# Kernel optimization log

Measured on AMD Instinct MI355X. Metric: run time of the kernel, lower is better.

Reference implementation:

```python
import jax, jax.numpy as jnp
import numpy as np

B, T, V, D, L, FFM = 2, 2048, 50257, 1024, 8, 2


def setup_inputs() -> dict:
    key = jax.random.key(0)
    ks = jax.random.split(key, 10)
    s = 0.02
    return {
        "input_ids": jax.random.randint(ks[0], (B, T), 0, V),
        "embed": jax.random.normal(ks[1], (V, D), jnp.float32) * s,
        "norm1_w": jnp.ones((L, D), jnp.float32),
        "norm2_w": jnp.ones((L, D), jnp.float32),
        "a_diag": jax.random.uniform(ks[2], (L, D), jnp.float32, 0.5, 0.99),
        "W_in": jax.random.normal(ks[3], (L, D, D), jnp.float32) * s,
        "b_in": jnp.zeros((L, D), jnp.float32),
        "W_out": jax.random.normal(ks[4], (L, D, D), jnp.float32) * s,
        "ff_w1": jax.random.normal(ks[5], (L, D, FFM * D), jnp.float32) * s,
        "ff_b1": jnp.zeros((L, FFM * D), jnp.float32),
        "ff_w2": jax.random.normal(ks[6], (L, FFM * D, D), jnp.float32) * s,
        "ff_b2": jnp.zeros((L, D), jnp.float32),
        "final_norm_w": jnp.ones((D,), jnp.float32),
        "lm_head_w": jax.random.normal(ks[7], (V, D), jnp.float32) * s,
    }


def rmsnorm(x, w, eps=1e-6):
    return x * jax.lax.rsqrt(jnp.mean(x * x, axis=-1, keepdims=True) + eps) * w


def chaos_core(x, a, Win, bin_, Wout):
    pre = jnp.einsum('btd,de->bte', x, Win) + bin_  # precompute input drive (parallel)

    def step(s, p):
        s = jnp.tanh(a * s + p)
        return s, s

    s0 = jnp.zeros((x.shape[0], x.shape[-1]), x.dtype)
    _, hs = jax.lax.scan(step, s0, jnp.swapaxes(pre, 0, 1))  # (T, B, D)
    hs = jnp.swapaxes(hs, 0, 1)  # (B, T, D)
    return jnp.einsum('btd,de->bte', hs, Wout)


def reference(input_ids, embed, norm1_w, norm2_w, a_diag, W_in, b_in, W_out,
              ff_w1, ff_b1, ff_w2, ff_b2, final_norm_w, lm_head_w):
    x = embed[input_ids]  # (B, T, D)
    for i in range(L):
        # input_norm -> core -> residual
        x = x + chaos_core(rmsnorm(x, norm1_w[i]), a_diag[i], W_in[i], b_in[i], W_out[i])
        # ff_norm -> FeedForward (Linear -> SiLU -> Linear) -> residual
        h = rmsnorm(x, norm2_w[i])
        h = jax.nn.silu(jnp.einsum('btd,df->btf', h, ff_w1[i]) + ff_b1[i])
        x = x + jnp.einsum('btf,fd->btd', h, ff_w2[i]) + ff_b2[i]
    x = rmsnorm(x, final_norm_w)
    return jnp.einsum('btd,vd->btv', x, lm_head_w)  # logits (B, T, V)
```

## Files before the change

kernel.cpp:

```cpp
#include <hip/hip_runtime.h>

typedef unsigned short u16;
typedef __bf16 bf16x8 __attribute__((ext_vector_type(8)));
typedef float f32x4 __attribute__((ext_vector_type(4)));
typedef unsigned short u16x4 __attribute__((ext_vector_type(4)));

__device__ __forceinline__ u16 f2bf(float f) {
  union { float f; unsigned int u; } v; v.f = f;
  return (u16)((v.u + 0x7FFFu + ((v.u >> 16) & 1u)) >> 16);
}

__device__ __forceinline__ void gload16(const void* g, void* l) {
  __builtin_amdgcn_global_load_lds(
      (const __attribute__((address_space(1))) unsigned int*)g,
      (__attribute__((address_space(3))) unsigned int*)l, 16, 0, 0);
}

__global__ void prep_weights(const float* __restrict__ Win,
                             const float* __restrict__ Wout,
                             const float* __restrict__ ffw1,
                             const float* __restrict__ ffw2,
                             u16* __restrict__ WinT, u16* __restrict__ WoutT,
                             u16* __restrict__ f1T, u16* __restrict__ f2T) {
  __shared__ float tile[32][33];
  const int tk = blockIdx.x;
  const float* src; u16* dst;
  int R, C, tr, tc;
  if (tk < 8192) {
    const int l = tk >> 10, rem = tk & 1023;
    R = 1024; C = 1024; tr = rem >> 5; tc = rem & 31;
    src = Win + (size_t)l * 1048576; dst = WinT + (size_t)l * 1048576;
  } else if (tk < 16384) {
    const int q = tk - 8192, l = q >> 10, rem = q & 1023;
    R = 1024; C = 1024; tr = rem >> 5; tc = rem & 31;
    src = Wout + (size_t)l * 1048576; dst = WoutT + (size_t)l * 1048576;
  } else if (tk < 32768) {
    const int q = tk - 16384, l = q >> 11, rem = q & 2047;
    R = 1024; C = 2048; tr = rem >> 6; tc = rem & 63;
    src = ffw1 + (size_t)l * 2097152; dst = f1T + (size_t)l * 2097152;
  } else {
    const int q = tk - 32768, l = q >> 11, rem = q & 2047;
    R = 2048; C = 1024; tr = rem >> 5; tc = rem & 31;
    src = ffw2 + (size_t)l * 2097152; dst = f2T + (size_t)l * 2097152;
  }
  const int tx = threadIdx.x, ty = threadIdx.y;
  const int c0 = tc * 32, r0 = tr * 32;
#pragma unroll
  for (int k = 0; k < 32; k += 8)
    tile[ty + k][tx] = src[(size_t)(r0 + ty + k) * C + (c0 + tx)];
  __syncthreads();
#pragma unroll
  for (int k = 0; k < 32; k += 8)
    dst[(size_t)(c0 + ty + k) * R + (r0 + tx)] = f2bf(tile[tx][ty + k]);
}

__global__ void lm_cast_kernel(const float* __restrict__ lm, u16* __restrict__ out) {
  const int row = blockIdx.x;
  const int t = threadIdx.x;
  u16x4 o = {0, 0, 0, 0};
  if (row < 50257) {
    float4 v = *(const float4*)(lm + (size_t)row * 1024 + t * 4);
    o.x = f2bf(v.x); o.y = f2bf(v.y); o.z = f2bf(v.z); o.w = f2bf(v.w);
  }
  *(u16x4*)(out + (size_t)row * 1024 + t * 4) = o;
}

__global__ void embed_kernel(const int* __restrict__ ids, const float* __restrict__ embed,
                             float* __restrict__ x) {
  const int row = blockIdx.x;
  const int id = ids[row];
  const int t = threadIdx.x;
  *(float4*)(x + (size_t)row * 1024 + t * 4) =
      *(const float4*)(embed + (size_t)id * 1024 + t * 4);
}

__global__ void rmsnorm_kernel(const float* __restrict__ x, const float* __restrict__ w,
                               u16* __restrict__ out) {
  const int row = blockIdx.x, tid = threadIdx.x;
  const float* xr = x + (size_t)row * 1024;
  float4 v = *(const float4*)(xr + tid * 4);
  float ss = v.x * v.x + v.y * v.y + v.z * v.z + v.w * v.w;
#pragma unroll
  for (int off = 32; off; off >>= 1) ss += __shfl_xor(ss, off);
  __shared__ float red[4];
  if ((tid & 63) == 0) red[tid >> 6] = ss;
  __syncthreads();
  const float tot = red[0] + red[1] + red[2] + red[3];
  const float r = rsqrtf(tot * (1.0f / 1024.0f) + 1e-6f);
  float4 wv = *(const float4*)(w + tid * 4);
  u16x4 o;
  o.x = f2bf(v.x * r * wv.x); o.y = f2bf(v.y * r * wv.y);
  o.z = f2bf(v.z * r * wv.z); o.w = f2bf(v.w * r * wv.w);
  *(u16x4*)(out + (size_t)row * 1024 + tid * 4) = o;
}

__device__ __forceinline__ void sload(const float* __restrict__ p, int tb,
                                      float A2b, float (&buf)[8]) {
#pragma unroll
  for (int j = 0; j < 8; j++)
    buf[j] = fmaf(p[(size_t)(tb + j) * 1024], 2.8853900817779268f, A2b);
}

__device__ __forceinline__ void scomp(float (&buf)[8], float m2A2, float& r,
                                      u16* __restrict__ o, int tb) {
#pragma unroll
  for (int j = 0; j < 8; j++) {
    float z = fmaf(m2A2, r, buf[j]);
    float e = __builtin_amdgcn_exp2f(z);
    r = __builtin_amdgcn_rcpf(1.0f + e);
    o[(size_t)(tb + j) * 1024] = f2bf(fmaf(-2.0f, r, 1.0f));
  }
}

__global__ __launch_bounds__(256) void scan_kernel(const float* __restrict__ pre,
                                                   const float* __restrict__ a_diag,
                                                   const float* __restrict__ b_in,
                                                   u16* __restrict__ hs) {
  const int T = 2048;
  const int idx = blockIdx.x * 256 + threadIdx.x;
  const int b = idx >> 10, d = idx & 1023;
  const float* p = pre + (size_t)b * T * 1024 + d;
  u16* o = hs + (size_t)b * T * 1024 + d;
  const float A2 = a_diag[d] * 2.8853900817779268f;
  const float A2b = fmaf(2.8853900817779268f, b_in[d], A2);
  const float m2A2 = -2.0f * A2;
  float r = 0.5f;
  float b0[8], b1[8], b2[8], b3[8];
  sload(p, 0, A2b, b0); sload(p, 8, A2b, b1);
  sload(p, 16, A2b, b2); sload(p, 24, A2b, b3);
  for (int t0 = 0; t0 < T; t0 += 32) {
    scomp(b0, m2A2, r, o, t0);
    if (t0 + 32 < T) sload(p, t0 + 32, A2b, b0);
    scomp(b1, m2A2, r, o, t0 + 8);
    if (t0 + 32 < T) sload(p, t0 + 40, A2b, b1);
    scomp(b2, m2A2, r, o, t0 + 16);
    if (t0 + 32 < T) sload(p, t0 + 48, A2b, b2);
    scomp(b3, m2A2, r, o, t0 + 24);
    if (t0 + 32 < T) sload(p, t0 + 56, A2b, b3);
  }
}

template <int EPI>
__global__ __launch_bounds__(256) void gemmL(
    const u16* __restrict__ A, int lda, const u16* __restrict__ Bw, int ldb,
    const float* __restrict__ bias, float* Cf, u16* __restrict__ Cb,
    int ldc, int K) {
  __shared__ char lds[73728];
  const int tid = threadIdx.x;
  const int lane = tid & 63;
  const int wc = tid >> 6;
  const int tm = blockIdx.y * 64, tn = blockIdx.x * 128;
  const int lr = lane & 15;
  const int sb0 = ((lane >> 4) ^ (lane & 7)) << 4;

  const int srow = tid >> 3;
  const int sxs = ((tid & 7) ^ (srow & 7)) << 4;
  const char* pA = (const char*)A + (size_t)(tm + srow) * lda * 2 + sxs;
  const char* pB = (const char*)Bw + (size_t)(tn + srow) * ldb * 2 + sxs;
  const size_t a32 = (size_t)lda * 64;
  const size_t b32 = (size_t)ldb * 64;

#define STGL(kt, bufo)                                \
  {                                                   \
    char* d = lds + (bufo) + tid * 16;                \
    const size_t kb = (size_t)(kt) << 7;              \
    gload16(pA + kb, d);                              \
    gload16(pA + a32 + kb, d + 4096);                 \
    gload16(pB + kb, d + 8192);                       \
    gload16(pB + b32 + kb, d + 12288);                \
    gload16(pB + 2 * b32 + kb, d + 16384);            \
    gload16(pB + 3 * b32 + kb, d + 20480);            \
  }

  f32x4 acc[4][2] = {};
  const int nkt = K >> 6;

  STGL(0, 0);
  STGL(1, 24576);
  int cb = 0;
  for (int kt = 0; kt < nkt; ++kt) {
    if (kt + 2 < nkt) {
      const int nb = cb + 49152 >= 73728 ? cb - 24576 : cb + 49152;
      STGL(kt + 2, nb);
      asm volatile("s_waitcnt vmcnt(12)" ::: "memory");
    } else if (kt + 1 < nkt) {
      asm volatile("s_waitcnt vmcnt(6)" ::: "memory");
    } else {
      asm volatile("s_waitcnt vmcnt(0)" ::: "memory");
    }
    __builtin_amdgcn_s_barrier();
    const char* base = lds + cb;
    bf16x8 aF[4][2], bF[2][2];
#pragma unroll
    for (int m = 0; m < 4; m++)
#pragma unroll
      for (int ks = 0; ks < 2; ks++)
        aF[m][ks] =
            *(const bf16x8*)(base + (m * 16 + lr) * 128 + (sb0 ^ (ks << 6)));
#pragma unroll
    for (int n = 0; n < 2; n++)
#pragma unroll
      for (int ks = 0; ks < 2; ks++)
        bF[n][ks] = *(const bf16x8*)(base + 8192 +
                                     (wc * 32 + n * 16 + lr) * 128 +
                                     (sb0 ^ (ks << 6)));
#pragma unroll
    for (int ks = 0; ks < 2; ks++)
#pragma unroll
      for (int m = 0; m < 4; m++)
#pragma unroll
        for (int n = 0; n < 2; n++)
          acc[m][n] = __builtin_amdgcn_mfma_f32_16x16x32_bf16(
              aF[m][ks], bF[n][ks], acc[m][n], 0, 0, 0);
    __builtin_amdgcn_s_barrier();
    cb = (cb + 24576 == 73728) ? 0 : cb + 24576;
  }
#undef STGL

  const int crow = tm + ((lane >> 4) << 2);
  const int ccol = tn + wc * 32 + lr;
#pragma unroll
  for (int m = 0; m < 4; m++) {
#pragma unroll
    for (int n = 0; n < 2; n++) {
      const int cg = ccol + n * 16;
      float bb = 0.0f;
      if (EPI == 2 || EPI == 3) bb = bias[cg];
#pragma unroll
      for (int j = 0; j < 4; j++) {
        const size_t off = (size_t)(crow + m * 16 + j) * ldc + cg;
        const float v = acc[m][n][j] + bb;
        if (EPI == 0) {
          Cf[off] = v;
        } else if (EPI == 1) {
          Cf[off] += v;
        } else if (EPI == 2) {
          const float sg = __builtin_amdgcn_rcpf(
              1.0f + __builtin_amdgcn_exp2f(-1.4426950408889634f * v));
          Cb[off] = f2bf(v * sg);
        } else {
          Cf[off] += v;
        }
      }
    }
  }
}

__global__ __launch_bounds__(512, 2) void gemm_lm8(
    const u16* __restrict__ A, const u16* __restrict__ Bw,
    float* __restrict__ C, int Nreal) {
  __shared__ char lds[131072];
  const int tid = threadIdx.x;
  const int lane = tid & 63;
  const int wid = tid >> 6;
  const int wr = wid >> 2;
  const int wc = wid & 3;
  const int bid = blockIdx.x;
  const int tm = (((bid & 7) << 1) + ((bid >> 3) & 1)) << 8;
  const int tn = (bid >> 4) << 8;

  const int srow = tid >> 3;
  const int sxor = ((tid & 7) ^ (srow & 7)) << 4;
  const char* pAs = (const char*)A + ((size_t)(tm + srow) << 11) + sxor;
  const char* pBs = (const char*)Bw + ((size_t)(tn + srow) << 11) + sxor;

#define STG(p, h, kt, ro)                                      \
  {                                                            \
    char* d = lds + (ro) + tid * 16;                           \
    const char* s = (p) + ((size_t)(h) << 18) + ((kt) << 7);   \
    gload16(s, d);                                             \
    gload16(s + (64ull << 11), d + 8192);                      \
  }

  const int lr = lane & 15;
  const int sb0 = (((lane >> 4) ^ (lane & 7)) << 4);
  const int sb[2] = {sb0, sb0 ^ 64};
  const int aB = wr * 16384 + lr * 128;
  const int bB = 32768 + (wc >> 1) * 16384 + ((wc & 1) * 64 + lr) * 128;

  bf16x8 aR[4][2], bR[2][2][2];
  f32x4 acc[8][4] = {};

#define LDA_Q(bufo, mq)                                                         \
  _Pragma("unroll") for (int m_ = 0; m_ < 4; m_++)                              \
  _Pragma("unroll") for (int k_ = 0; k_ < 2; k_++)                              \
      aR[m_][k_] = *(const bf16x8*)(lds + (bufo) + aB + (mq)*8192 + m_*2048 + sb[k_]);

#define LDB_Q(bufo, nq)                                                         \
  _Pragma("unroll") for (int n_ = 0; n_ < 2; n_++)                              \
  _Pragma("unroll") for (int k_ = 0; k_ < 2; k_++)                              \
      bR[nq][n_][k_] = *(const bf16x8*)(lds + (bufo) + bB + (nq)*4096 + n_*2048 + sb[k_]);

#define MFMA_Q(mq, nq)                                                          \
  __builtin_amdgcn_s_setprio(1);                                                \
  _Pragma("unroll") for (int m_ = 0; m_ < 4; m_++)                              \
  _Pragma("unroll") for (int n_ = 0; n_ < 2; n_++)                              \
  _Pragma("unroll") for (int k_ = 0; k_ < 2; k_++)                              \
      acc[(mq)*4 + m_][(nq)*2 + n_] = __builtin_amdgcn_mfma_f32_16x16x32_bf16(  \
          aR[m_][k_], bR[nq][n_][k_], acc[(mq)*4 + m_][(nq)*2 + n_], 0, 0, 0);  \
  __builtin_amdgcn_s_setprio(0);

#define BAR() __builtin_amdgcn_s_barrier()
#define LGKM0() asm volatile("s_waitcnt lgkmcnt(0)" ::: "memory")

  STG(pAs, 0, 0, 0);
  STG(pAs, 1, 0, 16384);
  STG(pBs, 0, 0, 32768);
  STG(pBs, 1, 0, 49152);
  STG(pBs, 0, 1, 65536 + 32768);
  STG(pBs, 1, 1, 65536 + 49152);
  asm volatile("s_waitcnt vmcnt(4)" ::: "memory");
  BAR();

  for (int it = 0; it < 8; ++it) {
    const int t1 = 2 * it + 1, t2 = 2 * it + 2, t3 = 2 * it + 3;
    const bool st = (it < 7);
    LDA_Q(0, 0); LDB_Q(0, 0);
    STG(pAs, 0, t1, 65536);
    BAR(); LGKM0(); MFMA_Q(0, 0); BAR();
    LDB_Q(0, 1);
    STG(pAs, 1, t1, 65536 + 16384);
    BAR(); LGKM0(); MFMA_Q(0, 1); BAR();
    LDA_Q(0, 1);
    if (st) STG(pBs, 0, t2, 32768);
    BAR(); LGKM0(); MFMA_Q(1, 0); BAR();
    if (st) STG(pBs, 1, t2, 49152);
    BAR(); LGKM0(); MFMA_Q(1, 1);
    if (st) { asm volatile("s_waitcnt vmcnt(4)" ::: "memory"); }
    else    { asm volatile("s_waitcnt vmcnt(0)" ::: "memory"); }
    BAR();
    LDA_Q(65536, 0); LDB_Q(65536, 0);
    if (st) STG(pAs, 0, t2, 0);
    BAR(); LGKM0(); MFMA_Q(0, 0); BAR();
    LDB_Q(65536, 1);
    if (st) STG(pAs, 1, t2, 16384);
    BAR(); LGKM0(); MFMA_Q(0, 1); BAR();
    LDA_Q(65536, 1);
    if (st) STG(pBs, 0, t3, 65536 + 32768);
    BAR(); LGKM0(); MFMA_Q(1, 0); BAR();
    if (st) STG(pBs, 1, t3, 65536 + 49152);
    BAR(); LGKM0(); MFMA_Q(1, 1);
    if (st) { asm volatile("s_waitcnt vmcnt(4)" ::: "memory"); }
    else    { asm volatile("s_waitcnt vmcnt(0)" ::: "memory"); }
    BAR();
  }
#undef STG
#undef LDA_Q
#undef LDB_Q
#undef MFMA_Q
#undef BAR
#undef LGKM0

  const int crow = tm + wr * 128 + ((lane >> 4) << 2);
  const int ccol = tn + wc * 64 + lr;
#pragma unroll
  for (int M_ = 0; M_ < 8; M_++) {
    const int r = crow + (M_ >> 2) * 64 + (M_ & 3) * 16;
#pragma unroll
    for (int N_ = 0; N_ < 4; N_++) {
      const int cg = ccol + (N_ >> 1) * 32 + (N_ & 1) * 16;
      if (cg < Nreal) {
#pragma unroll
        for (int j = 0; j < 4; j++)
          C[(size_t)(r + j) * Nreal + cg] = acc[M_][N_][j];
      }
    }
  }
}

extern "C" void kernel_launch(void* const* d_in, const int* in_sizes, int n_in,
                              void* d_out, int out_size, void* d_ws, size_t ws_size,
                              hipStream_t stream) {
  const int D = 1024, V = 50257, L = 8;
  const int M = 4096;
  const int Vpad = 50432;
  const size_t MD = (size_t)M * D;

  const int* ids = (const int*)d_in[0];
  const float* embedw = (const float*)d_in[1];
  const float* norm1_w = (const float*)d_in[2];
  const float* norm2_w = (const float*)d_in[3];
  const float* a_diag = (const float*)d_in[4];
  const float* W_in = (const float*)d_in[5];
  const float* b_in = (const float*)d_in[6];
  const float* W_out = (const float*)d_in[7];
  const float* ff_w1 = (const float*)d_in[8];
  const float* ff_b1 = (const float*)d_in[9];
  const float* ff_w2 = (const float*)d_in[10];
  const float* ff_b2 = (const float*)d_in[11];
  const float* final_norm_w = (const float*)d_in[12];
  const float* lm_head_w = (const float*)d_in[13];

  char* w = (char*)d_ws;
  float* x = (float*)w;   w += MD * 4;
  u16* h = (u16*)w;       w += MD * 2;
  float* pre = (float*)w; w += MD * 4;
  u16* hs = (u16*)w;      w += MD * 2;
  u16* hff = (u16*)w;     w += MD * 2 * 2;
  u16* WinT = (u16*)w;    w += (size_t)L * D * D * 2;
  u16* WoutT = (u16*)w;   w += (size_t)L * D * D * 2;
  u16* ffw1T = (u16*)w;   w += (size_t)L * 2 * D * D * 2;
  u16* ffw2T = (u16*)w;   w += (size_t)L * 2 * D * D * 2;
  u16* lmpad = (u16*)w;   w += (size_t)Vpad * D * 2;

  prep_weights<<<49152, dim3(32, 8), 0, stream>>>(
      W_in, W_out, ff_w1, ff_w2, WinT, WoutT, ffw1T, ffw2T);
  lm_cast_kernel<<<Vpad, 256, 0, stream>>>(lm_head_w, lmpad);
  embed_kernel<<<M, 256, 0, stream>>>(ids, embedw, x);

  for (int l = 0; l < L; l++) {
    rmsnorm_kernel<<<M, 256, 0, stream>>>(x, norm1_w + (size_t)l * D, h);
    gemmL<0><<<dim3(8, 64), 256, 0, stream>>>(
        h, D, WinT + (size_t)l * D * D, D, nullptr, pre, nullptr, D, D);
    scan_kernel<<<8, 256, 0, stream>>>(pre, a_diag + (size_t)l * D,
                                       b_in + (size_t)l * D, hs);
    gemmL<1><<<dim3(8, 64), 256, 0, stream>>>(
        hs, D, WoutT + (size_t)l * D * D, D, nullptr, x, nullptr, D, D);
    rmsnorm_kernel<<<M, 256, 0, stream>>>(x, norm2_w + (size_t)l * D, h);
    gemmL<2><<<dim3(16, 64), 256, 0, stream>>>(
        h, D, ffw1T + (size_t)l * 2 * D * D, D, ff_b1 + (size_t)l * 2 * D,
        nullptr, hff, 2 * D, D);
    gemmL<3><<<dim3(8, 64), 256, 0, stream>>>(
        hff, 2 * D, ffw2T + (size_t)l * 2 * D * D, 2 * D,
        ff_b2 + (size_t)l * D, x, nullptr, D, 2 * D);
  }

  rmsnorm_kernel<<<M, 256, 0, stream>>>(x, final_norm_w, h);
  gemm_lm8<<<dim3(8 * 394), 512, 0, stream>>>(h, lmpad, (float*)d_out, V);
}
```

Baseline: 2.712 ms.

## Fuse per-layer kernels into one persistent cooperative megakernel with grid syncs

Replaces the per-layer sequence of rmsnorm, GEMM and scan launches with a single cooperative kernel of 256 blocks. It runs the embedding, lm_head cast, norms, GEMMs with 128x128 tiles and the scan as phases separated by grid.sync. The aim is to remove many kernel launch gaps. In exchange, the GEMMs now use only 256 persistent blocks with double buffering, and the scan runs on 4 blocks while the rest wait at a barrier. The fallback gemmL also drops from triple to double buffering.

```diff
diff --git a/kernel.cpp b/kernel.cpp
--- a/kernel.cpp
+++ b/kernel.cpp
@@ -1,4 +1,7 @@
 #include <hip/hip_runtime.h>
+#include <hip/hip_cooperative_groups.h>
+
+namespace cg = cooperative_groups;
 
 typedef unsigned short u16;
 typedef __bf16 bf16x8 __attribute__((ext_vector_type(8)));
@@ -112,32 +115,35 @@
   }
 }
 
-__global__ __launch_bounds__(256) void scan_kernel(const float* __restrict__ pre,
-                                                   const float* __restrict__ a_diag,
-                                                   const float* __restrict__ b_in,
-                                                   u16* __restrict__ hs) {
-  const int T = 2048;
-  const int idx = blockIdx.x * 256 + threadIdx.x;
-  const int b = idx >> 10, d = idx & 1023;
-  const float* p = pre + (size_t)b * T * 1024 + d;
-  u16* o = hs + (size_t)b * T * 1024 + d;
-  const float A2 = a_diag[d] * 2.8853900817779268f;
-  const float A2b = fmaf(2.8853900817779268f, b_in[d], A2);
+__device__ __forceinline__ void scan_chain(const float* __restrict__ p,
+                                           u16* __restrict__ o, float A2,
+                                           float A2b) {
   const float m2A2 = -2.0f * A2;
   float r = 0.5f;
   float b0[8], b1[8], b2[8], b3[8];
   sload(p, 0, A2b, b0); sload(p, 8, A2b, b1);
   sload(p, 16, A2b, b2); sload(p, 24, A2b, b3);
-  for (int t0 = 0; t0 < T; t0 += 32) {
+  for (int t0 = 0; t0 < 2048; t0 += 32) {
     scomp(b0, m2A2, r, o, t0);
-    if (t0 + 32 < T) sload(p, t0 + 32, A2b, b0);
+    if (t0 + 32 < 2048) sload(p, t0 + 32, A2b, b0);
     scomp(b1, m2A2, r, o, t0 + 8);
-    if (t0 + 32 < T) sload(p, t0 + 40, A2b, b1);
+    if (t0 + 32 < 2048) sload(p, t0 + 40, A2b, b1);
     scomp(b2, m2A2, r, o, t0 + 16);
-    if (t0 + 32 < T) sload(p, t0 + 48, A2b, b2);
+    if (t0 + 32 < 2048) sload(p, t0 + 48, A2b, b2);
     scomp(b3, m2A2, r, o, t0 + 24);
-    if (t0 + 32 < T) sload(p, t0 + 56, A2b, b3);
-  }
+    if (t0 + 32 < 2048) sload(p, t0 + 56, A2b, b3);
+  }
+}
+
+__global__ __launch_bounds__(256) void scan_kernel(const float* __restrict__ pre,
+                                                   const float* __restrict__ a_diag,
+                                                   const float* __restrict__ b_in,
+                                                   u16* __restrict__ hs) {
+  const int idx = blockIdx.x * 256 + threadIdx.x;
+  const int b = idx >> 10, d = idx & 1023;
+  const float A2 = a_diag[d] * 2.8853900817779268f;
+  const float A2b = fmaf(2.8853900817779268f, b_in[d], A2);
+  scan_chain(pre + (size_t)b * 2097152 + d, hs + (size_t)b * 2097152 + d, A2, A2b);
 }
 
 template <int EPI>
@@ -145,7 +151,7 @@
     const u16* __restrict__ A, int lda, const u16* __restrict__ Bw, int ldb,
     const float* __restrict__ bias, float* Cf, u16* __restrict__ Cb,
     int ldc, int K) {
-  __shared__ char lds[73728];
+  __shared__ char lds[49152];
   const int tid = threadIdx.x;
   const int lane = tid & 63;
   const int wc = tid >> 6;
@@ -176,20 +182,16 @@
   const int nkt = K >> 6;
 
   STGL(0, 0);
-  STGL(1, 24576);
-  int cb = 0;
+  int cur = 0;
   for (int kt = 0; kt < nkt; ++kt) {
-    if (kt + 2 < nkt) {
-      const int nb = cb + 49152 >= 73728 ? cb - 24576 : cb + 49152;
-      STGL(kt + 2, nb);
-      asm volatile("s_waitcnt vmcnt(12)" ::: "memory");
-    } else if (kt + 1 < nkt) {
+    if (kt + 1 < nkt) {
+      STGL(kt + 1, (cur ^ 1) * 24576);
       asm volatile("s_waitcnt vmcnt(6)" ::: "memory");
     } else {
       asm volatile("s_waitcnt vmcnt(0)" ::: "memory");
     }
     __builtin_amdgcn_s_barrier();
-    const char* base = lds + cb;
+    const char* base = lds + cur * 24576;
     bf16x8 aF[4][2], bF[2][2];
 #pragma unroll
     for (int m = 0; m < 4; m++)
@@ -213,7 +215,7 @@
           acc[m][n] = __builtin_amdgcn_mfma_f32_16x16x32_bf16(
               aF[m][ks], bF[n][ks], acc[m][n], 0, 0, 0);
     __builtin_amdgcn_s_barrier();
-    cb = (cb + 24576 == 73728) ? 0 : cb + 24576;
+    cur ^= 1;
   }
 #undef STGL
 
@@ -244,6 +246,195 @@
       }
     }
   }
+}
+
+
+template <int EPI>
+__device__ __forceinline__ void gemm_phase(
+    char* lds, const u16* __restrict__ A, int lda,
+    const u16* __restrict__ B, int ldb, const float* __restrict__ bias,
+    float* __restrict__ Cf, u16* __restrict__ Cb, int ldc,
+    int ntm, int ntn, int K) {
+  const int tid = threadIdx.x;
+  const int lane = tid & 63;
+  const int wid = tid >> 6;
+  const int wr = wid >> 2, wc = wid & 3;
+  const int lr = lane & 15;
+  const int sb0 = ((lane >> 4) ^ (lane & 7)) << 4;
+  const int srow = tid >> 3;
+  const int sxs = ((tid & 7) ^ (srow & 7)) << 4;
+  const int nkt = K >> 6;
+  const int ntiles = ntm * ntn;
+
+  for (int t = blockIdx.x; t < ntiles; t += gridDim.x) {
+    const int tm = (t / ntn) << 7, tn = (t % ntn) << 7;
+    const char* pA = (const char*)A + (size_t)(tm + srow) * lda * 2 + sxs;
+    const char* pB = (const char*)B + (size_t)(tn + srow) * ldb * 2 + sxs;
+    const size_t pA2 = (size_t)lda << 7;
+    const size_t pB2 = (size_t)ldb << 7;
+    f32x4 acc[4][2] = {};
+    __syncthreads();
+    {
+      char* d = lds + tid * 16;
+      gload16(pA, d); gload16(pA + pA2, d + 8192);
+      gload16(pB, d + 16384); gload16(pB + pB2, d + 24576);
+    }
+    int cur = 0;
+    for (int kt = 0; kt < nkt; ++kt) {
+      if (kt + 1 < nkt) {
+        const size_t kb = (size_t)(kt + 1) << 7;
+        char* d = lds + (cur ^ 1) * 32768 + tid * 16;
+        gload16(pA + kb, d); gload16(pA + pA2 + kb, d + 8192);
+        gload16(pB + kb, d + 16384); gload16(pB + pB2 + kb, d + 24576);
+        asm volatile("s_waitcnt vmcnt(4)" ::: "memory");
+      } else {
+        asm volatile("s_waitcnt vmcnt(0)" ::: "memory");
+      }
+      __builtin_amdgcn_s_barrier();
+      const char* base = lds + cur * 32768;
+      bf16x8 aF[4][2], bF[2][2];
+#pragma unroll
+      for (int m = 0; m < 4; m++)
+#pragma unroll
+        for (int ks = 0; ks < 2; ks++)
+          aF[m][ks] = *(const bf16x8*)(base + (wr * 64 + m * 16 + lr) * 128 +
+                                       (sb0 ^ (ks << 6)));
+#pragma unroll
+      for (int n = 0; n < 2; n++)
+#pragma unroll
+        for (int ks = 0; ks < 2; ks++)
+          bF[n][ks] = *(const bf16x8*)(base + 16384 +
+                                       (wc * 32 + n * 16 + lr) * 128 +
+                                       (sb0 ^ (ks << 6)));
+#pragma unroll
+      for (int ks = 0; ks < 2; ks++)
+#pragma unroll
+        for (int m = 0; m < 4; m++)
+#pragma unroll
+          for (int n = 0; n < 2; n++)
+            acc[m][n] = __builtin_amdgcn_mfma_f32_16x16x32_bf16(
+                aF[m][ks], bF[n][ks], acc[m][n], 0, 0, 0);
+      __builtin_amdgcn_s_barrier();
+      cur ^= 1;
+    }
+    const int crow = tm + wr * 64 + ((lane >> 4) << 2);
+    const int ccol = tn + wc * 32 + lr;
+#pragma unroll
+    for (int m = 0; m < 4; m++) {
+#pragma unroll
+      for (int n = 0; n < 2; n++) {
+        const int cg = ccol + n * 16;
+#pragma unroll
+        for (int j = 0; j < 4; j++) {
+          const size_t off = (size_t)(crow + m * 16 + j) * ldc + cg;
+          const float v = acc[m][n][j];
+          if (EPI == 0) {
+            Cf[off] = v;
+          } else if (EPI == 1) {
+            Cf[off] += v;
+          } else if (EPI == 2) {
+            const float vb = v + bias[cg];
+            const float sg = __builtin_amdgcn_rcpf(
+                1.0f + __builtin_amdgcn_exp2f(-1.4426950408889634f * vb));
+            Cb[off] = f2bf(vb * sg);
+          } else {
+            Cf[off] += v + bias[cg];
+          }
+        }
+      }
+    }
+  }
+}
+
+__device__ __forceinline__ void norm_phase(const float* __restrict__ xg,
+                                           const float* __restrict__ w,
+                                           u16* __restrict__ hg,
+                                           volatile float* red) {
+  const int tid = threadIdx.x;
+  const int sub = tid >> 8, t = tid & 255;
+#pragma unroll 1
+  for (int i = 0; i < 8; i++) {
+    const int row = blockIdx.x * 16 + i * 2 + sub;
+    const size_t ro = (size_t)row * 1024 + t * 4;
+    float4 v = *(const float4*)(xg + ro);
+    float ss = v.x * v.x + v.y * v.y + v.z * v.z + v.w * v.w;
+#pragma unroll
+    for (int off = 32; off; off >>= 1) ss += __shfl_xor(ss, off);
+    __syncthreads();
+    if ((tid & 63) == 0) red[tid >> 6] = ss;
+    __syncthreads();
+    const float tot =
+        red[sub * 4] + red[sub * 4 + 1] + red[sub * 4 + 2] + red[sub * 4 + 3];
+    const float rr = rsqrtf(tot * (1.0f / 1024.0f) + 1e-6f);
+    float4 wv = *(const float4*)(w + t * 4);
+    u16x4 o;
+    o.x = f2bf(v.x * rr * wv.x); o.y = f2bf(v.y * rr * wv.y);
+    o.z = f2bf(v.z * rr * wv.z); o.w = f2bf(v.w * rr * wv.w);
+    *(u16x4*)(hg + ro) = o;
+  }
+}
+
+__global__ __launch_bounds__(512, 1) void mega(
+    const int* __restrict__ ids, const float* __restrict__ embedw,
+    const float* __restrict__ n1w, const float* __restrict__ n2w,
+    const float* __restrict__ adiag, const float* __restrict__ bin,
+    const float* __restrict__ fb1, const float* __restrict__ fb2,
+    const float* __restrict__ finw, const float* __restrict__ lmw,
+    float* __restrict__ x, u16* __restrict__ h, float* __restrict__ pre,
+    u16* __restrict__ hs, u16* __restrict__ hff,
+    const u16* __restrict__ WinT, const u16* __restrict__ WoutT,
+    const u16* __restrict__ f1T, const u16* __restrict__ f2T,
+    u16* __restrict__ lmpad) {
+  __shared__ char smem[65536];
+  __shared__ float red[16];
+  cg::grid_group grid = cg::this_grid();
+  const int bid = blockIdx.x;
+  const int tid = threadIdx.x;
+
+  for (int row = bid; row < 50432; row += 256) {
+    unsigned int o = 0;
+    if (row < 50257) {
+      float2 v = *(const float2*)(lmw + (size_t)row * 1024 + tid * 2);
+      o = (unsigned int)f2bf(v.x) | ((unsigned int)f2bf(v.y) << 16);
+    }
+    *(unsigned int*)(lmpad + (size_t)row * 1024 + tid * 2) = o;
+  }
+  for (int row = bid; row < 4096; row += 256) {
+    const float2 v =
+        *(const float2*)(embedw + (size_t)ids[row] * 1024 + tid * 2);
+    *(float2*)(x + (size_t)row * 1024 + tid * 2) = v;
+  }
+  grid.sync();
+
+  for (int l = 0; l < 8; ++l) {
+    norm_phase(x, n1w + l * 1024, h, red);
+    grid.sync();
+    gemm_phase<0>(smem, h, 1024, WinT + (size_t)l * 1048576, 1024, nullptr,
+                  pre, nullptr, 1024, 32, 8, 1024);
+    grid.sync();
+    if (bid < 4) {
+      const int idx = bid * 512 + tid;
+      const int b = idx >> 10, d = idx & 1023;
+      const float A2 = adiag[l * 1024 + d] * 2.8853900817779268f;
+      const float A2b = fmaf(2.8853900817779268f, bin[l * 1024 + d], A2);
+      scan_chain(pre + (size_t)b * 2097152 + d, hs + (size_t)b * 2097152 + d,
+                 A2, A2b);
+    }
+    grid.sync();
+    gemm_phase<1>(smem, hs, 1024, WoutT + (size_t)l * 1048576, 1024, nullptr,
+                  x, nullptr, 1024, 32, 8, 1024);
+    grid.sync();
+    norm_phase(x, n2w + l * 1024, h, red);
+    grid.sync();
+    gemm_phase<2>(smem, h, 1024, f1T + (size_t)l * 2097152, 1024,
+                  fb1 + l * 2048, nullptr, hff, 2048, 32, 16, 1024);
+    grid.sync();
+    gemm_phase<3>(smem, hff, 2048, f2T + (size_t)l * 2097152, 2048,
+                  fb2 + l * 1024, x, nullptr, 1024, 32, 8, 2048);
+    grid.sync();
+  }
+
+  norm_phase(x, finw, h, red);
 }
 
 __global__ __launch_bounds__(512, 2) void gemm_lm8(
@@ -405,26 +596,37 @@
 
   prep_weights<<<49152, dim3(32, 8), 0, stream>>>(
       W_in, W_out, ff_w1, ff_w2, WinT, WoutT, ffw1T, ffw2T);
-  lm_cast_kernel<<<Vpad, 256, 0, stream>>>(lm_head_w, lmpad);
-  embed_kernel<<<M, 256, 0, stream>>>(ids, embedw, x);
-
-  for (int l = 0; l < L; l++) {
-    rmsnorm_kernel<<<M, 256, 0, stream>>>(x, norm1_w + (size_t)l * D, h);
-    gemmL<0><<<dim3(8, 64), 256, 0, stream>>>(
-        h, D, WinT + (size_t)l * D * D, D, nullptr, pre, nullptr, D, D);
-    scan_kernel<<<8, 256, 0, stream>>>(pre, a_diag + (size_t)l * D,
-                                       b_in + (size_t)l * D, hs);
-    gemmL<1><<<dim3(8, 64), 256, 0, stream>>>(
-        hs, D, WoutT + (size_t)l * D * D, D, nullptr, x, nullptr, D, D);
-    rmsnorm_kernel<<<M, 256, 0, stream>>>(x, norm2_w + (size_t)l * D, h);
-    gemmL<2><<<dim3(16, 64), 256, 0, stream>>>(
-        h, D, ffw1T + (size_t)l * 2 * D * D, D, ff_b1 + (size_t)l * 2 * D,
-        nullptr, hff, 2 * D, D);
-    gemmL<3><<<dim3(8, 64), 256, 0, stream>>>(
-        hff, 2 * D, ffw2T + (size_t)l * 2 * D * D, 2 * D,
-        ff_b2 + (size_t)l * D, x, nullptr, D, 2 * D);
-  }
-
-  rmsnorm_kernel<<<M, 256, 0, stream>>>(x, final_norm_w, h);
+
+  void* args[] = {
+      (void*)&ids,  (void*)&embedw, (void*)&norm1_w, (void*)&norm2_w,
+      (void*)&a_diag, (void*)&b_in, (void*)&ff_b1,   (void*)&ff_b2,
+      (void*)&final_norm_w, (void*)&lm_head_w,
+      (void*)&x, (void*)&h, (void*)&pre, (void*)&hs, (void*)&hff,
+      (void*)&WinT, (void*)&WoutT, (void*)&ffw1T, (void*)&ffw2T,
+      (void*)&lmpad};
+  hipError_t err = hipLaunchCooperativeKernel((const void*)mega, dim3(256),
+                                              dim3(512), args, 0, stream);
+  if (err != hipSuccess) {
+    lm_cast_kernel<<<Vpad, 256, 0, stream>>>(lm_head_w, lmpad);
+    embed_kernel<<<M, 256, 0, stream>>>(ids, embedw, x);
+    for (int l = 0; l < L; l++) {
+      rmsnorm_kernel<<<M, 256, 0, stream>>>(x, norm1_w + (size_t)l * D, h);
+      gemmL<0><<<dim3(8, 64), 256, 0, stream>>>(
+          h, D, WinT + (size_t)l * D * D, D, nullptr, pre, nullptr, D, D);
+      scan_kernel<<<8, 256, 0, stream>>>(pre, a_diag + (size_t)l * D,
+                                         b_in + (size_t)l * D, hs);
+      gemmL<1><<<dim3(8, 64), 256, 0, stream>>>(
+          hs, D, WoutT + (size_t)l * D * D, D, nullptr, x, nullptr, D, D);
+      rmsnorm_kernel<<<M, 256, 0, stream>>>(x, norm2_w + (size_t)l * D, h);
+      gemmL<2><<<dim3(16, 64), 256, 0, stream>>>(
+          h, D, ffw1T + (size_t)l * 2 * D * D, D, ff_b1 + (size_t)l * 2 * D,
+          nullptr, hff, 2 * D, D);
+      gemmL<3><<<dim3(8, 64), 256, 0, stream>>>(
+          hff, 2 * D, ffw2T + (size_t)l * 2 * D * D, 2 * D,
+          ff_b2 + (size_t)l * D, x, nullptr, D, 2 * D);
+    }
+    rmsnorm_kernel<<<M, 256, 0, stream>>>(x, final_norm_w, h);
+  }
+
   gemm_lm8<<<dim3(8 * 394), 512, 0, stream>>>(h, lmpad, (float*)d_out, V);
 }
```

After: 5.971 ms. +120.2%, slower.

## Merge prep kernels into one launch and switch GEMM to double-buffered LDS

Applied to the files above, without the earlier changes.

Three setup kernels (the weight transpose-casts, the lm_head cast and the embedding gather) are merged into a single launch that dispatches on block index, removing two launch gaps. The layer GEMM goes from a 3-stage to a 2-stage LDS pipeline, cutting shared memory per block from 72KB to 48KB so more blocks can be resident per CU. The cost is less prefetch depth, so more global-load latency may be exposed within each block.

```diff
diff --git a/kernel.cpp b/kernel.cpp
--- a/kernel.cpp
+++ b/kernel.cpp
@@ -16,14 +16,36 @@
       (__attribute__((address_space(3))) unsigned int*)l, 16, 0, 0);
 }
 
-__global__ void prep_weights(const float* __restrict__ Win,
-                             const float* __restrict__ Wout,
-                             const float* __restrict__ ffw1,
-                             const float* __restrict__ ffw2,
-                             u16* __restrict__ WinT, u16* __restrict__ WoutT,
-                             u16* __restrict__ f1T, u16* __restrict__ f2T) {
+__global__ __launch_bounds__(256) void prep_all(
+    const float* __restrict__ Win, const float* __restrict__ Wout,
+    const float* __restrict__ ffw1, const float* __restrict__ ffw2,
+    u16* __restrict__ WinT, u16* __restrict__ WoutT,
+    u16* __restrict__ f1T, u16* __restrict__ f2T,
+    const float* __restrict__ lmw, u16* __restrict__ lmpad,
+    const int* __restrict__ ids, const float* __restrict__ embedw,
+    float* __restrict__ x) {
   __shared__ float tile[32][33];
-  const int tk = blockIdx.x;
+  const int bid = blockIdx.x;
+  const int tid = threadIdx.x;
+
+  if (bid >= 49152 + 50432) {
+    const int row = bid - (49152 + 50432);
+    *(float4*)(x + (size_t)row * 1024 + tid * 4) =
+        *(const float4*)(embedw + (size_t)ids[row] * 1024 + tid * 4);
+    return;
+  }
+  if (bid >= 49152) {
+    const int row = bid - 49152;
+    u16x4 o = {0, 0, 0, 0};
+    if (row < 50257) {
+      float4 v = *(const float4*)(lmw + (size_t)row * 1024 + tid * 4);
+      o.x = f2bf(v.x); o.y = f2bf(v.y); o.z = f2bf(v.z); o.w = f2bf(v.w);
+    }
+    *(u16x4*)(lmpad + (size_t)row * 1024 + tid * 4) = o;
+    return;
+  }
+
+  const int tk = bid;
   const float* src; u16* dst;
   int R, C, tr, tc;
   if (tk < 8192) {
@@ -43,7 +65,7 @@
     R = 2048; C = 1024; tr = rem >> 5; tc = rem & 31;
     src = ffw2 + (size_t)l * 2097152; dst = f2T + (size_t)l * 2097152;
   }
-  const int tx = threadIdx.x, ty = threadIdx.y;
+  const int tx = tid & 31, ty = tid >> 5;
   const int c0 = tc * 32, r0 = tr * 32;
 #pragma unroll
   for (int k = 0; k < 32; k += 8)
@@ -52,26 +74,6 @@
 #pragma unroll
   for (int k = 0; k < 32; k += 8)
     dst[(size_t)(c0 + ty + k) * R + (r0 + tx)] = f2bf(tile[tx][ty + k]);
-}
-
-__global__ void lm_cast_kernel(const float* __restrict__ lm, u16* __restrict__ out) {
-  const int row = blockIdx.x;
-  const int t = threadIdx.x;
-  u16x4 o = {0, 0, 0, 0};
-  if (row < 50257) {
-    float4 v = *(const float4*)(lm + (size_t)row * 1024 + t * 4);
-    o.x = f2bf(v.x); o.y = f2bf(v.y); o.z = f2bf(v.z); o.w = f2bf(v.w);
-  }
-  *(u16x4*)(out + (size_t)row * 1024 + t * 4) = o;
-}
-
-__global__ void embed_kernel(const int* __restrict__ ids, const float* __restrict__ embed,
-                             float* __restrict__ x) {
-  const int row = blockIdx.x;
-  const int id = ids[row];
-  const int t = threadIdx.x;
-  *(float4*)(x + (size_t)row * 1024 + t * 4) =
-      *(const float4*)(embed + (size_t)id * 1024 + t * 4);
 }
 
 __global__ void rmsnorm_kernel(const float* __restrict__ x, const float* __restrict__ w,
@@ -145,7 +147,7 @@
     const u16* __restrict__ A, int lda, const u16* __restrict__ Bw, int ldb,
     const float* __restrict__ bias, float* Cf, u16* __restrict__ Cb,
     int ldc, int K) {
-  __shared__ char lds[73728];
+  __shared__ char lds[49152];
   const int tid = threadIdx.x;
   const int lane = tid & 63;
   const int wc = tid >> 6;
@@ -176,20 +178,16 @@
   const int nkt = K >> 6;
 
   STGL(0, 0);
-  STGL(1, 24576);
-  int cb = 0;
+  int cur = 0;
   for (int kt = 0; kt < nkt; ++kt) {
-    if (kt + 2 < nkt) {
-      const int nb = cb + 49152 >= 73728 ? cb - 24576 : cb + 49152;
-      STGL(kt + 2, nb);
-      asm volatile("s_waitcnt vmcnt(12)" ::: "memory");
-    } else if (kt + 1 < nkt) {
+    if (kt + 1 < nkt) {
+      STGL(kt + 1, (cur ^ 1) * 24576);
       asm volatile("s_waitcnt vmcnt(6)" ::: "memory");
     } else {
       asm volatile("s_waitcnt vmcnt(0)" ::: "memory");
     }
     __builtin_amdgcn_s_barrier();
-    const char* base = lds + cb;
+    const char* base = lds + cur * 24576;
     bf16x8 aF[4][2], bF[2][2];
 #pragma unroll
     for (int m = 0; m < 4; m++)
@@ -213,7 +211,7 @@
           acc[m][n] = __builtin_amdgcn_mfma_f32_16x16x32_bf16(
               aF[m][ks], bF[n][ks], acc[m][n], 0, 0, 0);
     __builtin_amdgcn_s_barrier();
-    cb = (cb + 24576 == 73728) ? 0 : cb + 24576;
+    cur ^= 1;
   }
 #undef STGL
 
@@ -403,10 +401,9 @@
   u16* ffw2T = (u16*)w;   w += (size_t)L * 2 * D * D * 2;
   u16* lmpad = (u16*)w;   w += (size_t)Vpad * D * 2;
 
-  prep_weights<<<49152, dim3(32, 8), 0, stream>>>(
-      W_in, W_out, ff_w1, ff_w2, WinT, WoutT, ffw1T, ffw2T);
-  lm_cast_kernel<<<Vpad, 256, 0, stream>>>(lm_head_w, lmpad);
-  embed_kernel<<<M, 256, 0, stream>>>(ids, embedw, x);
+  prep_all<<<49152 + Vpad + M, 256, 0, stream>>>(
+      W_in, W_out, ff_w1, ff_w2, WinT, WoutT, ffw1T, ffw2T,
+      lm_head_w, lmpad, ids, embedw, x);
 
   for (int l = 0; l < L; l++) {
     rmsnorm_kernel<<<M, 256, 0, stream>>>(x, norm1_w + (size_t)l * D, h);
```

New measurement: 2.703 ms, median of 2. No clear change (-0.3%).
